# Kernel tuning notes

Hardware: AMD Instinct MI355X
Metric: run time of the kernel (lower is better)

The kernel has to match this reference:

```python
import jax, jax.numpy as jnp
import numpy as np

B, S, H = 4, 2048, 1024
N_EXPERTS = 8
EXPERT_DIM = 1024  # must equal H (see module: wo features = expert_dim, output added to zeros_like(x))
TOP_K = 2
Z_LOSS_COEF = 0.001


def setup_inputs() -> dict:
    key = jax.random.key(0)
    ks = jax.random.split(key, 8)
    s_h = 1.0 / np.sqrt(H)
    s_e = 1.0 / np.sqrt(EXPERT_DIM)
    return {
        "x": jax.random.normal(ks[0], (B, S, H), dtype=jnp.float32),
        "router_w": jax.random.normal(ks[1], (H, N_EXPERTS), dtype=jnp.float32) * s_h,
        "router_b": jnp.zeros((N_EXPERTS,), dtype=jnp.float32),
        "wi_w": jax.random.normal(ks[2], (N_EXPERTS, H, EXPERT_DIM), dtype=jnp.float32) * s_h,
        "wi_b": jnp.zeros((N_EXPERTS, EXPERT_DIM), dtype=jnp.float32),
        "wo_w": jax.random.normal(ks[3], (N_EXPERTS, EXPERT_DIM, EXPERT_DIM), dtype=jnp.float32) * s_e,
        "wo_b": jnp.zeros((N_EXPERTS, EXPERT_DIM), dtype=jnp.float32),
    }


def reference(x, router_w, router_b, wi_w, wi_b, wo_w, wo_b):
    # Router (deterministic=True: no jitter noise, no dropout)
    logits = jnp.einsum("bsh,he->bse", x, router_w) + router_b        # [B,S,Ne]
    probs = jax.nn.softmax(logits, axis=-1)
    z_loss = jnp.mean(jnp.square(jax.nn.logsumexp(logits, axis=-1))) * Z_LOSS_COEF
    topk_p, topk_i = jax.lax.top_k(probs, TOP_K)                      # [B,S,2]
    topk_p = topk_p / jnp.sum(topk_p, axis=-1, keepdims=True)
    # Faithful to source: mask[...,None] ([B,S,2,1]) broadcasts against x ([B,S,H])
    # producing [B,S,2,H]; combined output has that shape.
    out = jnp.zeros((B, S, TOP_K, H), dtype=x.dtype)
    n_experts = wi_w.shape[0]
    for e in range(n_experts):  # fixed small expert loop, as in source
        mask = (topk_i == e)                                          # [B,S,2]
        p = jnp.where(mask, topk_p, 0.0)                              # [B,S,2]
        xin = jnp.where(mask[..., None], x[:, :, None, :], 0.0)       # [B,S,2,H]
        h = jax.nn.gelu(jnp.einsum("bskh,hd->bskd", xin, wi_w[e]) + wi_b[e])
        y = jnp.einsum("bskd,do->bsko", h, wo_w[e]) + wo_b[e]         # [B,S,2,H]
        out = out + y * p[..., None]
    return out, z_loss
```

## Files before the change

### kernel.cpp

```cpp
#include <hip/hip_runtime.h>

typedef unsigned short u16;
typedef unsigned int   u32;
typedef __bf16 bf16x8 __attribute__((ext_vector_type(8)));
typedef float  f32x4  __attribute__((ext_vector_type(4)));

#define NTOK   8192
#define NSLOT  16384

#define XB_OFF   0UL
#define WIT_OFF  16777216UL
#define WOT_OFF  33554432UL
#define HB_OFF   50331648UL
#define RE_OFF   83886080UL
#define RP_OFF   83951616UL
#define SEG_OFF  84017152UL
#define META_OFF 84082688UL
#define ZB_OFF   (META_OFF + 4096UL)
#define WS_NEED  (ZB_OFF + 32768UL)

__device__ __forceinline__ u16 f2b(float f) {
  u32 u = __float_as_uint(f);
  u32 r = (u + 0x7fffu + ((u >> 16) & 1u)) >> 16;
  return (u16)r;
}

__device__ __forceinline__ void async_cp16(const void* g, void* l) {
  __builtin_amdgcn_global_load_lds(
      (const __attribute__((address_space(1))) u32*)g,
      (__attribute__((address_space(3))) u32*)l, 16, 0, 0);
}

__device__ __forceinline__ float gelu_f(float v) {
  float u  = 0.7978845608028654f * (v + 0.044715f * v * v * v);
  float ex = __expf(2.0f * u);
  float th = 1.0f - 2.0f / (ex + 1.0f);
  return 0.5f * v * (1.0f + th);
}

__global__ __launch_bounds__(256) void k_transpose(const float* __restrict__ wi,
                                                   const float* __restrict__ wo,
                                                   u16* __restrict__ wit,
                                                   u16* __restrict__ wot) {
  __shared__ float t[64][65];
  int z = blockIdx.z;
  int e = z & 7;
  const float* src = ((z < 8) ? wi : wo) + ((size_t)e << 20);
  u16* dst = ((z < 8) ? wit : wot) + ((size_t)e << 20);
  int h0 = blockIdx.y * 64, d0 = blockIdx.x * 64;
  int tid = threadIdx.x;
#pragma unroll
  for (int j = 0; j < 4; j++) {
    int f = tid + 256 * j;
    int r = f >> 4, c4 = f & 15;
    float4 v = *(const float4*)&src[(size_t)(h0 + r) * 1024 + d0 + c4 * 4];
    t[r][c4 * 4 + 0] = v.x; t[r][c4 * 4 + 1] = v.y;
    t[r][c4 * 4 + 2] = v.z; t[r][c4 * 4 + 3] = v.w;
  }
  __syncthreads();
#pragma unroll
  for (int j = 0; j < 4; j++) {
    int f = tid + 256 * j;
    int d = f >> 4, c4 = f & 15;
    u32 p0 = (u32)f2b(t[c4 * 4 + 0][d]) | ((u32)f2b(t[c4 * 4 + 1][d]) << 16);
    u32 p1 = (u32)f2b(t[c4 * 4 + 2][d]) | ((u32)f2b(t[c4 * 4 + 3][d]) << 16);
    u32* dp = (u32*)&dst[(size_t)(d0 + d) * 1024 + h0 + c4 * 4];
    dp[0] = p0; dp[1] = p1;
  }
}

__global__ __launch_bounds__(256) void k_router(const float* __restrict__ x,
    const float* __restrict__ rw, const float* __restrict__ rb,
    u16* __restrict__ xb, int* __restrict__ route_e, float* __restrict__ route_p,
    float* __restrict__ zbuf) {
  int wv = blockIdx.x * 4 + (threadIdx.x >> 6);
  int l = threadIdx.x & 63;
#pragma unroll 1
  for (int t = 0; t < 4; t++) {
    int tok = wv * 4 + t;
    const float* xrow = x + (size_t)tok * 1024;
    u16* xbrow = xb + (size_t)tok * 1024;
    float a[8] = {0.f, 0.f, 0.f, 0.f, 0.f, 0.f, 0.f, 0.f};
#pragma unroll
    for (int j = 0; j < 16; j++) {
      int c = j * 64 + l;
      float xj = xrow[c];
      xbrow[c] = f2b(xj);
      float4 w0 = *(const float4*)&rw[c * 8];
      float4 w1 = *(const float4*)&rw[c * 8 + 4];
      a[0] += xj * w0.x; a[1] += xj * w0.y; a[2] += xj * w0.z; a[3] += xj * w0.w;
      a[4] += xj * w1.x; a[5] += xj * w1.y; a[6] += xj * w1.z; a[7] += xj * w1.w;
    }
#pragma unroll
    for (int e = 0; e < 8; e++)
#pragma unroll
      for (int off = 32; off; off >>= 1) a[e] += __shfl_xor(a[e], off, 64);
    if (l == 0) {
#pragma unroll
      for (int e = 0; e < 8; e++) a[e] += rb[e];
      int e0 = 0; float b0 = a[0];
#pragma unroll
      for (int k = 1; k < 8; k++) if (a[k] > b0) { b0 = a[k]; e0 = k; }
      int e1 = -1; float b1 = -3.4e38f;
#pragma unroll
      for (int k = 0; k < 8; k++) { if (k == e0) continue; if (a[k] > b1) { b1 = a[k]; e1 = k; } }
      float s = 0.f;
#pragma unroll
      for (int k = 0; k < 8; k++) s += __expf(a[k] - b0);
      float lse = b0 + __logf(s);
      float q1 = __expf(b1 - b0);
      route_e[tok * 2 + 0] = e0; route_e[tok * 2 + 1] = e1;
      route_p[tok * 2 + 0] = 1.0f / (1.0f + q1);
      route_p[tok * 2 + 1] = q1 / (1.0f + q1);
      zbuf[tok] = lse * lse;
    }
  }
}

__global__ __launch_bounds__(256) void k_scan(
    const int* __restrict__ route_e, int* __restrict__ offs,
    int* __restrict__ cursors, int* __restrict__ ntiles,
    int* __restrict__ tile_e, int* __restrict__ tile_r0,
    const float* __restrict__ zbuf, float* __restrict__ zout) {
  __shared__ int cnt[8];
  __shared__ float zs[4];
  int tid = threadIdx.x;
  if (tid < 8) cnt[tid] = 0;
  __syncthreads();
  for (int i = tid; i < NSLOT; i += 256) atomicAdd(&cnt[route_e[i]], 1);
  float z = 0.f;
  for (int i = tid; i < NTOK; i += 256) z += zbuf[i];
#pragma unroll
  for (int off = 32; off; off >>= 1) z += __shfl_xor(z, off, 64);
  if ((tid & 63) == 0) zs[tid >> 6] = z;
  __syncthreads();
  if (tid == 0) {
    *zout = (zs[0] + zs[1] + zs[2] + zs[3]) * (0.001f / 8192.0f);
    int o = 0, nt = 0;
    offs[0] = 0;
    for (int e = 0; e < 8; e++) {
      int c = cnt[e];
      cursors[e] = o;
      for (int r = 0; r < c; r += 320) { tile_e[nt] = e; tile_r0[nt] = o + r; nt++; }
      o += c;
      offs[e + 1] = o;
    }
    *ntiles = nt;
  }
}

__global__ __launch_bounds__(256) void k_scatter(const int* __restrict__ route_e,
                                                 int* __restrict__ cursors,
                                                 int* __restrict__ seg) {
  int i = blockIdx.x * 256 + threadIdx.x;
  int e = route_e[i];
  int lane = threadIdx.x & 63;
#pragma unroll
  for (int ex = 0; ex < 8; ex++) {
    unsigned long long mask = __ballot(e == ex);
    if (e == ex) {
      int cnt = __popcll(mask);
      int leader = __ffsll((long long)mask) - 1;
      int base = 0;
      if (lane == leader) base = atomicAdd(&cursors[ex], cnt);
      base = __shfl(base, leader, 64);
      int rank = __popcll(mask & ((1ull << lane) - 1ull));
      seg[base + rank] = i;
    }
  }
}


#define BAR()    asm volatile("s_barrier" ::: "memory")
#define WAITV0() asm volatile("s_waitcnt vmcnt(0)" ::: "memory")

#define STAGE_A(B, KT, J) async_cp16(asrc[J] + (KT) * 64, &As[B][(w * 40 + (J) * 8) * 64])
#define STAGE_B(B, KT, J) async_cp16(bsrc[J] + (KT) * 64, &Bs[B][(w * 32 + (J) * 8) * 64])

#define PHASE(CUR, Q)                                                              \
  do {                                                                             \
    bf16x8 af[2][2], bfr[2][4];                                                    \
    _Pragma("unroll")                                                              \
    for (int kk = 0; kk < 2; kk++) {                                               \
      int c = ((kk * 4 + rh) ^ (rl & 7)) * 8;                                      \
      _Pragma("unroll")                                                            \
      for (int d = 0; d < 2; d++)                                                  \
        af[kk][d] = *(const bf16x8*)&As[CUR][(wr * 160 + (2 * (Q) + d) * 16 + rl) * 64 + c]; \
      _Pragma("unroll")                                                            \
      for (int n = 0; n < 4; n++)                                                  \
        bfr[kk][n] = *(const bf16x8*)&Bs[CUR][(wc * 64 + n * 16 + rl) * 64 + c];   \
    }                                                                              \
    __builtin_amdgcn_s_setprio(1);                                                 \
    _Pragma("unroll")                                                              \
    for (int kk = 0; kk < 2; kk++)                                                 \
      _Pragma("unroll")                                                            \
      for (int d = 0; d < 2; d++)                                                  \
        _Pragma("unroll")                                                          \
        for (int n = 0; n < 4; n++)                                                \
          acc[2 * (Q) + d][n] = __builtin_amdgcn_mfma_f32_16x16x32_bf16(           \
              af[kk][d], bfr[kk][n], acc[2 * (Q) + d][n], 0, 0, 0);                \
    __builtin_amdgcn_s_setprio(0);                                                 \
  } while (0)

#define GEMM_BODY()                                                                \
  _Pragma("unroll")                                                                \
  for (int j = 0; j < 5; j++) STAGE_A(0, 0, j);                                    \
  _Pragma("unroll")                                                                \
  for (int j = 0; j < 4; j++) STAGE_B(0, 0, j);                                    \
  WAITV0(); BAR();                                                                 \
  _Pragma("unroll 2")                                                              \
  for (int g = 0; g < 16; g++) {                                                   \
    int cur = g & 1, nxt = cur ^ 1;                                                \
    bool pf = (g < 15);                                                            \
    if (pf) { STAGE_A(nxt, g + 1, 0); STAGE_A(nxt, g + 1, 1); STAGE_A(nxt, g + 1, 2); \
              STAGE_B(nxt, g + 1, 0); STAGE_B(nxt, g + 1, 1); }                    \
    PHASE(cur, 0); BAR();                                                          \
    if (pf) { STAGE_A(nxt, g + 1, 3); STAGE_A(nxt, g + 1, 4);                      \
              STAGE_B(nxt, g + 1, 2); STAGE_B(nxt, g + 1, 3); }                    \
    PHASE(cur, 1); BAR();                                                          \
    PHASE(cur, 2); BAR();                                                          \
    PHASE(cur, 3); BAR();                                                          \
    PHASE(cur, 4);                                                                 \
    WAITV0(); BAR();                                                               \
  }

__global__ __launch_bounds__(512, 2) void k_gemm_h(
    const u16* __restrict__ xb, const u16* __restrict__ wit, const float* __restrict__ wib,
    u16* __restrict__ hb, const int* __restrict__ seg, const int* __restrict__ offs,
    const int* __restrict__ tile_e, const int* __restrict__ tile_r0,
    const int* __restrict__ ntiles) {
  __shared__ u16 As[2][320 * 64];
  __shared__ u16 Bs[2][256 * 64];
  int bid = blockIdx.x;
  int swz = (bid & 7) * 30 + (bid >> 3);
  int mt = swz >> 2;
  if (mt >= *ntiles) return;
  int n0 = (swz & 3) << 8;
  int e = tile_e[mt], r0 = tile_r0[mt], end = offs[e + 1];
  int tid = threadIdx.x;
  int w = tid >> 6, l = tid & 63;
  int lr = l >> 3, lc = l & 7;
  int cs = lc ^ lr;
  const u16* asrc[5];
  const u16* bsrc[4];
#pragma unroll
  for (int j = 0; j < 5; j++) {
    int gr = r0 + w * 40 + j * 8 + lr;
    int idx = seg[(gr < end) ? gr : r0];
    asrc[j] = xb + (size_t)(idx >> 1) * 1024 + cs * 8;
  }
#pragma unroll
  for (int j = 0; j < 4; j++)
    bsrc[j] = wit + ((size_t)e << 20) + (size_t)(n0 + w * 32 + j * 8 + lr) * 1024 + cs * 8;
  f32x4 acc[10][4];
  f32x4 z4 = {0.f, 0.f, 0.f, 0.f};
#pragma unroll
  for (int m = 0; m < 10; m++)
#pragma unroll
    for (int n = 0; n < 4; n++) acc[m][n] = z4;
  int wr = w >> 2, wc = w & 3;
  int rl = l & 15, rh = l >> 4;
  GEMM_BODY()
#pragma unroll
  for (int n = 0; n < 4; n++) {
    int col = n0 + wc * 64 + n * 16 + rl;
    float bias = wib[e * 1024 + col];
#pragma unroll
    for (int m = 0; m < 10; m++) {
      int rbase = r0 + wr * 160 + m * 16 + rh * 4;
#pragma unroll
      for (int j = 0; j < 4; j++) {
        int gr = rbase + j;
        if (gr < end)
          hb[(size_t)gr * 1024 + col] = f2b(gelu_f(acc[m][n][j] + bias));
      }
    }
  }
}

__global__ __launch_bounds__(512, 2) void k_gemm_o(
    const u16* __restrict__ hb, const u16* __restrict__ wot, const float* __restrict__ wob,
    float* __restrict__ out, const int* __restrict__ seg, const int* __restrict__ offs,
    const int* __restrict__ tile_e, const int* __restrict__ tile_r0,
    const int* __restrict__ ntiles, const float* __restrict__ route_p) {
  __shared__ u16 As[2][320 * 64];
  __shared__ u16 Bs[2][256 * 64];
  int bid = blockIdx.x;
  int swz = (bid & 7) * 30 + (bid >> 3);
  int mt = swz >> 2;
  if (mt >= *ntiles) return;
  int n0 = (swz & 3) << 8;
  int e = tile_e[mt], r0 = tile_r0[mt], end = offs[e + 1];
  int tid = threadIdx.x;
  int w = tid >> 6, l = tid & 63;
  int lr = l >> 3, lc = l & 7;
  int cs = lc ^ lr;
  const u16* asrc[5];
  const u16* bsrc[4];
#pragma unroll
  for (int j = 0; j < 5; j++) {
    int gr = r0 + w * 40 + j * 8 + lr;
    int grc = (gr < end) ? gr : r0;
    asrc[j] = hb + (size_t)grc * 1024 + cs * 8;
  }
#pragma unroll
  for (int j = 0; j < 4; j++)
    bsrc[j] = wot + ((size_t)e << 20) + (size_t)(n0 + w * 32 + j * 8 + lr) * 1024 + cs * 8;
  f32x4 acc[10][4];
  f32x4 z4 = {0.f, 0.f, 0.f, 0.f};
#pragma unroll
  for (int m = 0; m < 10; m++)
#pragma unroll
    for (int n = 0; n < 4; n++) acc[m][n] = z4;
  int wr = w >> 2, wc = w & 3;
  int rl = l & 15, rh = l >> 4;
  GEMM_BODY()
#pragma unroll
  for (int m = 0; m < 10; m++) {
    int rbase = r0 + wr * 160 + m * 16 + rh * 4;
#pragma unroll
    for (int j = 0; j < 4; j++) {
      int gr = rbase + j;
      if (gr >= end) continue;
      int idx = seg[gr];
      float p = route_p[idx];
      float* orow = out + (size_t)idx * 1024;
#pragma unroll
      for (int n = 0; n < 4; n++) {
        int col = n0 + wc * 64 + n * 16 + rl;
        orow[col] = (acc[m][n][j] + wob[e * 1024 + col]) * p;
      }
    }
  }
}

extern "C" void kernel_launch(void* const* d_in, const int* in_sizes, int n_in,
                              void* d_out, int out_size, void* d_ws, size_t ws_size,
                              hipStream_t stream) {
  if (ws_size < WS_NEED) return;
  const float* x   = (const float*)d_in[0];
  const float* rw  = (const float*)d_in[1];
  const float* rb  = (const float*)d_in[2];
  const float* wiw = (const float*)d_in[3];
  const float* wib = (const float*)d_in[4];
  const float* wow = (const float*)d_in[5];
  const float* wob = (const float*)d_in[6];
  float* out = (float*)d_out;
  char* ws = (char*)d_ws;

  u16*   xb      = (u16*)(ws + XB_OFF);
  u16*   wit     = (u16*)(ws + WIT_OFF);
  u16*   wot     = (u16*)(ws + WOT_OFF);
  u16*   hb      = (u16*)(ws + HB_OFF);
  int*   route_e = (int*)(ws + RE_OFF);
  float* route_p = (float*)(ws + RP_OFF);
  int*   seg     = (int*)(ws + SEG_OFF);
  int*   offs    = (int*)(ws + META_OFF + 64);
  int*   cursors = (int*)(ws + META_OFF + 128);
  int*   ntiles  = (int*)(ws + META_OFF + 192);
  int*   tile_e  = (int*)(ws + META_OFF + 256);
  int*   tile_r0 = (int*)(ws + META_OFF + 1024);
  float* zbuf    = (float*)(ws + ZB_OFF);

  k_transpose<<<dim3(16, 16, 16), 256, 0, stream>>>(wiw, wow, wit, wot);
  k_router<<<512, 256, 0, stream>>>(x, rw, rb, xb, route_e, route_p, zbuf);
  k_scan<<<1, 256, 0, stream>>>(route_e, offs, cursors, ntiles, tile_e, tile_r0,
                                zbuf, out + (out_size - 1));
  k_scatter<<<64, 256, 0, stream>>>(route_e, cursors, seg);
  k_gemm_h<<<240, 512, 0, stream>>>(xb, wit, wib, hb, seg, offs,
                                    tile_e, tile_r0, ntiles);
  k_gemm_o<<<240, 512, 0, stream>>>(hb, wot, wob, out, seg, offs,
                                    tile_e, tile_r0, ntiles, route_p);
}
```

Measured before the change: 223.6 us.

## Merge prep kernels, fold scatter into scan, simplify GEMM main loop

Weight transpose and router run as one launch, so the separate transpose and router launches become a single kernel. The scatter step moves into the single-block scan kernel, with cursors kept in shared memory and per-wave counts reduced before the atomics, which removes one launch and a global-atomic stage. The GEMM inner loop now issues all async stages for the next k-tile at once and then runs one large MFMA block per half-k with a single barrier, replacing the five phased sub-steps with interleaved prefetch and setprio. This raises register pressure (10 A fragments live at once), and the scatter now runs serially inside one block.

```diff
diff --git a/kernel.cpp b/kernel.cpp
--- a/kernel.cpp
+++ b/kernel.cpp
@@ -38,101 +38,110 @@
   return 0.5f * v * (1.0f + th);
 }
 
-__global__ __launch_bounds__(256) void k_transpose(const float* __restrict__ wi,
-                                                   const float* __restrict__ wo,
-                                                   u16* __restrict__ wit,
-                                                   u16* __restrict__ wot) {
-  __shared__ float t[64][65];
-  int z = blockIdx.z;
-  int e = z & 7;
-  const float* src = ((z < 8) ? wi : wo) + ((size_t)e << 20);
-  u16* dst = ((z < 8) ? wit : wot) + ((size_t)e << 20);
-  int h0 = blockIdx.y * 64, d0 = blockIdx.x * 64;
+__global__ __launch_bounds__(256) void k_prep(const float* __restrict__ wi,
+    const float* __restrict__ wo, u16* __restrict__ wit, u16* __restrict__ wot,
+    const float* __restrict__ x, const float* __restrict__ rw,
+    const float* __restrict__ rb, u16* __restrict__ xb,
+    int* __restrict__ route_e, float* __restrict__ route_p,
+    float* __restrict__ zbuf) {
+  int bid = blockIdx.x;
   int tid = threadIdx.x;
-#pragma unroll
-  for (int j = 0; j < 4; j++) {
-    int f = tid + 256 * j;
-    int r = f >> 4, c4 = f & 15;
-    float4 v = *(const float4*)&src[(size_t)(h0 + r) * 1024 + d0 + c4 * 4];
-    t[r][c4 * 4 + 0] = v.x; t[r][c4 * 4 + 1] = v.y;
-    t[r][c4 * 4 + 2] = v.z; t[r][c4 * 4 + 3] = v.w;
-  }
-  __syncthreads();
-#pragma unroll
-  for (int j = 0; j < 4; j++) {
-    int f = tid + 256 * j;
-    int d = f >> 4, c4 = f & 15;
-    u32 p0 = (u32)f2b(t[c4 * 4 + 0][d]) | ((u32)f2b(t[c4 * 4 + 1][d]) << 16);
-    u32 p1 = (u32)f2b(t[c4 * 4 + 2][d]) | ((u32)f2b(t[c4 * 4 + 3][d]) << 16);
-    u32* dp = (u32*)&dst[(size_t)(d0 + d) * 1024 + h0 + c4 * 4];
-    dp[0] = p0; dp[1] = p1;
-  }
-}
-
-__global__ __launch_bounds__(256) void k_router(const float* __restrict__ x,
-    const float* __restrict__ rw, const float* __restrict__ rb,
-    u16* __restrict__ xb, int* __restrict__ route_e, float* __restrict__ route_p,
-    float* __restrict__ zbuf) {
-  int wv = blockIdx.x * 4 + (threadIdx.x >> 6);
-  int l = threadIdx.x & 63;
+  if (bid < 4096) {
+    __shared__ float t[64][65];
+    int e = (bid >> 8) & 7;
+    const float* src = ((bid < 2048) ? wi : wo) + ((size_t)e << 20);
+    u16* dst = ((bid < 2048) ? wit : wot) + ((size_t)e << 20);
+    int h0 = ((bid >> 4) & 15) * 64, d0 = (bid & 15) * 64;
+#pragma unroll
+    for (int j = 0; j < 4; j++) {
+      int f = tid + 256 * j;
+      int r = f >> 4, c4 = f & 15;
+      float4 v = *(const float4*)&src[(size_t)(h0 + r) * 1024 + d0 + c4 * 4];
+      t[r][c4 * 4 + 0] = v.x; t[r][c4 * 4 + 1] = v.y;
+      t[r][c4 * 4 + 2] = v.z; t[r][c4 * 4 + 3] = v.w;
+    }
+    __syncthreads();
+#pragma unroll
+    for (int j = 0; j < 4; j++) {
+      int f = tid + 256 * j;
+      int d = f >> 4, c4 = f & 15;
+      u32 p0 = (u32)f2b(t[c4 * 4 + 0][d]) | ((u32)f2b(t[c4 * 4 + 1][d]) << 16);
+      u32 p1 = (u32)f2b(t[c4 * 4 + 2][d]) | ((u32)f2b(t[c4 * 4 + 3][d]) << 16);
+      u32* dp = (u32*)&dst[(size_t)(d0 + d) * 1024 + h0 + c4 * 4];
+      dp[0] = p0; dp[1] = p1;
+    }
+  } else {
+    int wv = (bid - 4096) * 4 + (tid >> 6);
+    int l = tid & 63;
 #pragma unroll 1
-  for (int t = 0; t < 4; t++) {
-    int tok = wv * 4 + t;
-    const float* xrow = x + (size_t)tok * 1024;
-    u16* xbrow = xb + (size_t)tok * 1024;
-    float a[8] = {0.f, 0.f, 0.f, 0.f, 0.f, 0.f, 0.f, 0.f};
-#pragma unroll
-    for (int j = 0; j < 16; j++) {
-      int c = j * 64 + l;
-      float xj = xrow[c];
-      xbrow[c] = f2b(xj);
-      float4 w0 = *(const float4*)&rw[c * 8];
-      float4 w1 = *(const float4*)&rw[c * 8 + 4];
-      a[0] += xj * w0.x; a[1] += xj * w0.y; a[2] += xj * w0.z; a[3] += xj * w0.w;
-      a[4] += xj * w1.x; a[5] += xj * w1.y; a[6] += xj * w1.z; a[7] += xj * w1.w;
-    }
-#pragma unroll
-    for (int e = 0; e < 8; e++)
-#pragma unroll
-      for (int off = 32; off; off >>= 1) a[e] += __shfl_xor(a[e], off, 64);
-    if (l == 0) {
-#pragma unroll
-      for (int e = 0; e < 8; e++) a[e] += rb[e];
-      int e0 = 0; float b0 = a[0];
-#pragma unroll
-      for (int k = 1; k < 8; k++) if (a[k] > b0) { b0 = a[k]; e0 = k; }
-      int e1 = -1; float b1 = -3.4e38f;
-#pragma unroll
-      for (int k = 0; k < 8; k++) { if (k == e0) continue; if (a[k] > b1) { b1 = a[k]; e1 = k; } }
-      float s = 0.f;
-#pragma unroll
-      for (int k = 0; k < 8; k++) s += __expf(a[k] - b0);
-      float lse = b0 + __logf(s);
-      float q1 = __expf(b1 - b0);
-      route_e[tok * 2 + 0] = e0; route_e[tok * 2 + 1] = e1;
-      route_p[tok * 2 + 0] = 1.0f / (1.0f + q1);
-      route_p[tok * 2 + 1] = q1 / (1.0f + q1);
-      zbuf[tok] = lse * lse;
+    for (int t4 = 0; t4 < 4; t4++) {
+      int tok = wv * 4 + t4;
+      const float* xrow = x + (size_t)tok * 1024;
+      u16* xbrow = xb + (size_t)tok * 1024;
+      float a[8] = {0.f, 0.f, 0.f, 0.f, 0.f, 0.f, 0.f, 0.f};
+#pragma unroll
+      for (int j = 0; j < 16; j++) {
+        int c = j * 64 + l;
+        float xj = xrow[c];
+        xbrow[c] = f2b(xj);
+        float4 w0 = *(const float4*)&rw[c * 8];
+        float4 w1 = *(const float4*)&rw[c * 8 + 4];
+        a[0] += xj * w0.x; a[1] += xj * w0.y; a[2] += xj * w0.z; a[3] += xj * w0.w;
+        a[4] += xj * w1.x; a[5] += xj * w1.y; a[6] += xj * w1.z; a[7] += xj * w1.w;
+      }
+#pragma unroll
+      for (int e = 0; e < 8; e++)
+#pragma unroll
+        for (int off = 32; off; off >>= 1) a[e] += __shfl_xor(a[e], off, 64);
+      if (l == 0) {
+#pragma unroll
+        for (int e = 0; e < 8; e++) a[e] += rb[e];
+        int e0 = 0; float b0 = a[0];
+#pragma unroll
+        for (int k = 1; k < 8; k++) if (a[k] > b0) { b0 = a[k]; e0 = k; }
+        int e1 = -1; float b1 = -3.4e38f;
+#pragma unroll
+        for (int k = 0; k < 8; k++) { if (k == e0) continue; if (a[k] > b1) { b1 = a[k]; e1 = k; } }
+        float s = 0.f;
+#pragma unroll
+        for (int k = 0; k < 8; k++) s += __expf(a[k] - b0);
+        float lse = b0 + __logf(s);
+        float q1 = __expf(b1 - b0);
+        route_e[tok * 2 + 0] = e0; route_e[tok * 2 + 1] = e1;
+        route_p[tok * 2 + 0] = 1.0f / (1.0f + q1);
+        route_p[tok * 2 + 1] = q1 / (1.0f + q1);
+        zbuf[tok] = lse * lse;
+      }
     }
   }
 }
 
 __global__ __launch_bounds__(256) void k_scan(
     const int* __restrict__ route_e, int* __restrict__ offs,
-    int* __restrict__ cursors, int* __restrict__ ntiles,
-    int* __restrict__ tile_e, int* __restrict__ tile_r0,
-    const float* __restrict__ zbuf, float* __restrict__ zout) {
+    int* __restrict__ ntiles, int* __restrict__ tile_e, int* __restrict__ tile_r0,
+    int* __restrict__ seg, const float* __restrict__ zbuf, float* __restrict__ zout) {
   __shared__ int cnt[8];
+  __shared__ int curs[8];
   __shared__ float zs[4];
   int tid = threadIdx.x;
+  int lane = tid & 63;
   if (tid < 8) cnt[tid] = 0;
   __syncthreads();
-  for (int i = tid; i < NSLOT; i += 256) atomicAdd(&cnt[route_e[i]], 1);
+  int lc[8] = {0, 0, 0, 0, 0, 0, 0, 0};
+  for (int i = tid; i < NSLOT; i += 256) lc[route_e[i]]++;
+#pragma unroll
+  for (int e = 0; e < 8; e++)
+#pragma unroll
+    for (int off = 32; off; off >>= 1) lc[e] += __shfl_xor(lc[e], off, 64);
+  if (lane == 0) {
+#pragma unroll
+    for (int e = 0; e < 8; e++) atomicAdd(&cnt[e], lc[e]);
+  }
   float z = 0.f;
   for (int i = tid; i < NTOK; i += 256) z += zbuf[i];
 #pragma unroll
   for (int off = 32; off; off >>= 1) z += __shfl_xor(z, off, 64);
-  if ((tid & 63) == 0) zs[tid >> 6] = z;
+  if (lane == 0) zs[tid >> 6] = z;
   __syncthreads();
   if (tid == 0) {
     *zout = (zs[0] + zs[1] + zs[2] + zs[3]) * (0.001f / 8192.0f);
@@ -140,32 +149,28 @@
     offs[0] = 0;
     for (int e = 0; e < 8; e++) {
       int c = cnt[e];
-      cursors[e] = o;
+      curs[e] = o;
       for (int r = 0; r < c; r += 320) { tile_e[nt] = e; tile_r0[nt] = o + r; nt++; }
       o += c;
       offs[e + 1] = o;
     }
     *ntiles = nt;
   }
-}
-
-__global__ __launch_bounds__(256) void k_scatter(const int* __restrict__ route_e,
-                                                 int* __restrict__ cursors,
-                                                 int* __restrict__ seg) {
-  int i = blockIdx.x * 256 + threadIdx.x;
-  int e = route_e[i];
-  int lane = threadIdx.x & 63;
-#pragma unroll
-  for (int ex = 0; ex < 8; ex++) {
-    unsigned long long mask = __ballot(e == ex);
-    if (e == ex) {
-      int cnt = __popcll(mask);
-      int leader = __ffsll((long long)mask) - 1;
-      int base = 0;
-      if (lane == leader) base = atomicAdd(&cursors[ex], cnt);
-      base = __shfl(base, leader, 64);
-      int rank = __popcll(mask & ((1ull << lane) - 1ull));
-      seg[base + rank] = i;
+  __syncthreads();
+  for (int i = tid; i < NSLOT; i += 256) {
+    int e = route_e[i];
+#pragma unroll
+    for (int ex = 0; ex < 8; ex++) {
+      unsigned long long mask = __ballot(e == ex);
+      if (e == ex) {
+        int n = __popcll(mask);
+        int leader = __ffsll((long long)mask) - 1;
+        int base = 0;
+        if (lane == leader) base = atomicAdd(&curs[ex], n);
+        base = __shfl(base, leader, 64);
+        int rank = __popcll(mask & ((1ull << lane) - 1ull));
+        seg[base + rank] = i;
+      }
     }
   }
 }
@@ -177,50 +182,38 @@
 #define STAGE_A(B, KT, J) async_cp16(asrc[J] + (KT) * 64, &As[B][(w * 40 + (J) * 8) * 64])
 #define STAGE_B(B, KT, J) async_cp16(bsrc[J] + (KT) * 64, &Bs[B][(w * 32 + (J) * 8) * 64])
 
-#define PHASE(CUR, Q)                                                              \
-  do {                                                                             \
-    bf16x8 af[2][2], bfr[2][4];                                                    \
+#define STAGE_ALL(B, KT)                                                 \
+  do {                                                                   \
+    STAGE_A(B, KT, 0); STAGE_A(B, KT, 1); STAGE_A(B, KT, 2);             \
+    STAGE_A(B, KT, 3); STAGE_A(B, KT, 4);                                \
+    STAGE_B(B, KT, 0); STAGE_B(B, KT, 1); STAGE_B(B, KT, 2);             \
+    STAGE_B(B, KT, 3);                                                   \
+  } while (0)
+
+#define GEMM_BODY()                                                                \
+  STAGE_ALL(0, 0);                                                                 \
+  WAITV0(); BAR();                                                                 \
+  _Pragma("unroll 2")                                                              \
+  for (int g = 0; g < 16; g++) {                                                   \
+    int cur = g & 1;                                                               \
+    if (g < 15) STAGE_ALL(cur ^ 1, g + 1);                                         \
     _Pragma("unroll")                                                              \
     for (int kk = 0; kk < 2; kk++) {                                               \
       int c = ((kk * 4 + rh) ^ (rl & 7)) * 8;                                      \
-      _Pragma("unroll")                                                            \
-      for (int d = 0; d < 2; d++)                                                  \
-        af[kk][d] = *(const bf16x8*)&As[CUR][(wr * 160 + (2 * (Q) + d) * 16 + rl) * 64 + c]; \
+      bf16x8 af[10], bfr[4];                                                       \
       _Pragma("unroll")                                                            \
       for (int n = 0; n < 4; n++)                                                  \
-        bfr[kk][n] = *(const bf16x8*)&Bs[CUR][(wc * 64 + n * 16 + rl) * 64 + c];   \
-    }                                                                              \
-    __builtin_amdgcn_s_setprio(1);                                                 \
-    _Pragma("unroll")                                                              \
-    for (int kk = 0; kk < 2; kk++)                                                 \
+        bfr[n] = *(const bf16x8*)&Bs[cur][(wc * 64 + n * 16 + rl) * 64 + c];       \
       _Pragma("unroll")                                                            \
-      for (int d = 0; d < 2; d++)                                                  \
+      for (int m = 0; m < 10; m++)                                                 \
+        af[m] = *(const bf16x8*)&As[cur][(wr * 160 + m * 16 + rl) * 64 + c];       \
+      _Pragma("unroll")                                                            \
+      for (int m = 0; m < 10; m++)                                                 \
         _Pragma("unroll")                                                          \
         for (int n = 0; n < 4; n++)                                                \
-          acc[2 * (Q) + d][n] = __builtin_amdgcn_mfma_f32_16x16x32_bf16(           \
-              af[kk][d], bfr[kk][n], acc[2 * (Q) + d][n], 0, 0, 0);                \
-    __builtin_amdgcn_s_setprio(0);                                                 \
-  } while (0)
-
-#define GEMM_BODY()                                                                \
-  _Pragma("unroll")                                                                \
-  for (int j = 0; j < 5; j++) STAGE_A(0, 0, j);                                    \
-  _Pragma("unroll")                                                                \
-  for (int j = 0; j < 4; j++) STAGE_B(0, 0, j);                                    \
-  WAITV0(); BAR();                                                                 \
-  _Pragma("unroll 2")                                                              \
-  for (int g = 0; g < 16; g++) {                                                   \
-    int cur = g & 1, nxt = cur ^ 1;                                                \
-    bool pf = (g < 15);                                                            \
-    if (pf) { STAGE_A(nxt, g + 1, 0); STAGE_A(nxt, g + 1, 1); STAGE_A(nxt, g + 1, 2); \
-              STAGE_B(nxt, g + 1, 0); STAGE_B(nxt, g + 1, 1); }                    \
-    PHASE(cur, 0); BAR();                                                          \
-    if (pf) { STAGE_A(nxt, g + 1, 3); STAGE_A(nxt, g + 1, 4);                      \
-              STAGE_B(nxt, g + 1, 2); STAGE_B(nxt, g + 1, 3); }                    \
-    PHASE(cur, 1); BAR();                                                          \
-    PHASE(cur, 2); BAR();                                                          \
-    PHASE(cur, 3); BAR();                                                          \
-    PHASE(cur, 4);                                                                 \
+          acc[m][n] = __builtin_amdgcn_mfma_f32_16x16x32_bf16(af[m], bfr[n],       \
+                                                              acc[m][n], 0, 0, 0); \
+    }                                                                              \
     WAITV0(); BAR();                                                               \
   }
 
@@ -356,17 +349,15 @@
   float* route_p = (float*)(ws + RP_OFF);
   int*   seg     = (int*)(ws + SEG_OFF);
   int*   offs    = (int*)(ws + META_OFF + 64);
-  int*   cursors = (int*)(ws + META_OFF + 128);
   int*   ntiles  = (int*)(ws + META_OFF + 192);
   int*   tile_e  = (int*)(ws + META_OFF + 256);
   int*   tile_r0 = (int*)(ws + META_OFF + 1024);
   float* zbuf    = (float*)(ws + ZB_OFF);
 
-  k_transpose<<<dim3(16, 16, 16), 256, 0, stream>>>(wiw, wow, wit, wot);
-  k_router<<<512, 256, 0, stream>>>(x, rw, rb, xb, route_e, route_p, zbuf);
-  k_scan<<<1, 256, 0, stream>>>(route_e, offs, cursors, ntiles, tile_e, tile_r0,
-                                zbuf, out + (out_size - 1));
-  k_scatter<<<64, 256, 0, stream>>>(route_e, cursors, seg);
+  k_prep<<<4608, 256, 0, stream>>>(wiw, wow, wit, wot, x, rw, rb, xb,
+                                   route_e, route_p, zbuf);
+  k_scan<<<1, 256, 0, stream>>>(route_e, offs, ntiles, tile_e, tile_r0,
+                                seg, zbuf, out + (out_size - 1));
   k_gemm_h<<<240, 512, 0, stream>>>(xb, wit, wib, hb, seg, offs,
                                     tile_e, tile_r0, ntiles);
   k_gemm_o<<<240, 512, 0, stream>>>(hb, wot, wob, out, seg, offs,
```

New measurement: 332.6 us. +48.8%, slower.
